# Kernel optimization log

Measured on AMD Instinct MI355X. Metric: run time of the kernel, lower is better.

Reference implementation:

```python
import jax, jax.numpy as jnp
import numpy as np

D_MODEL = 96
D_STATE = 6
D_CONV = 9
D_INNER = 2 * D_MODEL          # expand = 2
DT_RANK = (D_MODEL + 15) // 16  # ceil(d_model/16) = 6
DIM_IN = 64
DIM_OUT = 64
BATCH = 16
SEQLEN = 4096


def setup_inputs() -> dict:
    key = jax.random.key(0)
    ks = jax.random.split(key, 12)
    def s(k, shape, scale=0.02):
        return jax.random.normal(k, shape, jnp.float32) * scale
    return {
        "x": jax.random.normal(ks[0], (BATCH, SEQLEN, D_MODEL), jnp.float32),
        # Mamba block params
        "in_proj_w": s(ks[1], (2 * D_INNER, D_MODEL)),
        "conv_w": s(ks[2], (D_INNER, D_CONV), 0.1),   # depthwise conv kernel
        "conv_b": jnp.zeros((D_INNER,), jnp.float32),
        "x_proj_w": s(ks[3], (DT_RANK + 2 * D_STATE, D_INNER)),
        "dt_proj_w": s(ks[4], (D_INNER, DT_RANK), 0.1),
        "dt_proj_b": s(ks[5], (D_INNER,), 0.1),
        "A_log": jnp.log(jnp.tile(jnp.arange(1, D_STATE + 1, dtype=jnp.float32), (D_INNER, 1))),
        "D_param": jnp.ones((D_INNER,), jnp.float32),
        "out_proj_w": s(ks[6], (D_MODEL, D_INNER)),
        "norm_w": jnp.ones((D_MODEL,), jnp.float32),  # RMSNorm weight
        # heads
        "out_fc_w": s(ks[7], (DIM_IN, D_MODEL)),
        "out_fc_b": jnp.zeros((DIM_IN,), jnp.float32),
        "mu_w": s(ks[8], (DIM_OUT, DIM_IN)),
        "mu_b": jnp.zeros((DIM_OUT,), jnp.float32),
        "sigma_w": s(ks[9], (DIM_OUT, DIM_IN)),
        "sigma_b": jnp.zeros((DIM_OUT,), jnp.float32),
    }


def _mamba_block(x, in_proj_w, conv_w, conv_b, x_proj_w, dt_proj_w, dt_proj_b,
                 A_log, D_param, out_proj_w):
    Bsz = x.shape[0]
    xz = jnp.einsum('bld,ed->ble', x, in_proj_w)          # (B,L,2*ED)
    xs, z = jnp.split(xz, 2, axis=-1)
    # causal depthwise conv1d (torch pads d_conv-1 both sides then trims right)
    xt = xs.transpose(0, 2, 1)                            # (B,ED,L)
    kern = conv_w[:, None, :]                             # (ED,1,K)
    xc = jax.lax.conv_general_dilated(xt, kern, window_strides=(1,),
                                      padding=[(D_CONV - 1, 0)],
                                      feature_group_count=D_INNER)
    xc = (xc + conv_b[None, :, None]).transpose(0, 2, 1)  # (B,L,ED)
    xc = jax.nn.silu(xc)
    dbc = jnp.einsum('ble,fe->blf', xc, x_proj_w)         # (B,L,dt_rank+2N)
    delta_r = dbc[..., :DT_RANK]
    Bm = dbc[..., DT_RANK:DT_RANK + D_STATE]              # (B,L,N)
    Cm = dbc[..., DT_RANK + D_STATE:]                     # (B,L,N)
    delta = jax.nn.softplus(jnp.einsum('blr,er->ble', delta_r, dt_proj_w) + dt_proj_b)
    A = -jnp.exp(A_log)                                   # (ED,N)
    deltaA = jnp.exp(delta[..., None] * A)                # (B,L,ED,N)
    BX = (delta * xc)[..., None] * Bm[:, :, None, :]      # (B,L,ED,N)

    def step(h, inputs):
        dA, bx = inputs
        h = dA * h + bx
        return h, h

    h0 = jnp.zeros((Bsz, D_INNER, D_STATE), x.dtype)
    _, hs = jax.lax.scan(step, h0, (deltaA.swapaxes(0, 1), BX.swapaxes(0, 1)))
    y = jnp.einsum('lben,bln->ble', hs, Cm)               # (B,L,ED)
    y = y + D_param * xc
    y = y * jax.nn.silu(z)
    return jnp.einsum('ble,de->bld', y, out_proj_w)       # (B,L,D)


def reference(x, in_proj_w, conv_w, conv_b, x_proj_w, dt_proj_w, dt_proj_b,
              A_log, D_param, out_proj_w, norm_w,
              out_fc_w, out_fc_b, mu_w, mu_b, sigma_w, sigma_b):
    # residual block: x + mixer(RMSNorm(x))   (dropout is identity at eval)
    h = x * jax.lax.rsqrt(jnp.mean(x * x, axis=-1, keepdims=True) + 1e-5) * norm_w
    out = x + _mamba_block(h, in_proj_w, conv_w, conv_b, x_proj_w,
                           dt_proj_w, dt_proj_b, A_log, D_param, out_proj_w)
    e = out.mean(axis=1)                                  # (B,D)
    feat = jax.nn.elu(jnp.tanh(e @ out_fc_w.T + out_fc_b))
    mu = feat @ mu_w.T + mu_b
    sigma = jax.nn.elu(feat @ sigma_w.T + sigma_b) + 1.0 + 1e-14
    return (feat, mu, sigma)
```

## Files before the change

### kernel.cpp

```cpp
#include <hip/hip_runtime.h>
#include <math.h>

#define BATCH 16
#define SEQLEN 4096
#define D_MODEL 96
#define D_STATE 6
#define D_CONV 9
#define D_INNER 192
#define DT_RANK 6
#define NPOS (BATCH * SEQLEN)

#define NC2 128
#define CT2 (SEQLEN / NC2)
#define NSEG 16
#define CPS (NC2 / NSEG)

#define OFF_XS    0L
#define OFF_Z     (OFF_XS   + (long)NPOS * 96)
#define OFF_OUT4  (OFF_Z    + (long)NPOS * 96)
#define OFF_SEG   (OFF_OUT4 + (long)BATCH * NC2 * 5 * 192 * 4)
#define OFF_XPART (OFF_SEG  + (long)BATCH * NSEG * 5 * 192 * 4)

typedef short v8s __attribute__((ext_vector_type(8)));
typedef float v4f __attribute__((ext_vector_type(4)));

__device__ __forceinline__ float silu_fast(float v) {
    return __fdividef(v, 1.0f + __expf(-v));
}
__device__ __forceinline__ float softplus_fast(float v) {
    return (v > 20.0f) ? v : __logf(1.0f + __expf(v));
}
__device__ __forceinline__ float eluf(float v) {
    return (v > 0.0f) ? v : expm1f(v);
}
__device__ __forceinline__ unsigned int pack_bf16(float a, float b) {
    unsigned int ua = __float_as_uint(a), ub = __float_as_uint(b);
    ua += 0x7FFFu + ((ua >> 16) & 1u);
    ub += 0x7FFFu + ((ub >> 16) & 1u);
    return (ua >> 16) | (ub & 0xFFFF0000u);
}
__device__ __forceinline__ unsigned short bf16h(float v) {
    unsigned int u = __float_as_uint(v);
    u += 0x7FFFu + ((u >> 16) & 1u);
    return (unsigned short)(u >> 16);
}
__device__ __forceinline__ float bf2f(unsigned short h) {
    return __uint_as_float(((unsigned int)h) << 16);
}

#define TP1 64
__global__ __launch_bounds__(256, 2) void k1_rmsnorm_inproj(
    const float* __restrict__ x, const float* __restrict__ W,
    const float* __restrict__ norm_w,
    unsigned short* __restrict__ xs, unsigned short* __restrict__ z,
    float* __restrict__ xpart)
{
    __shared__ unsigned int s_ovl[7680];
    __shared__ unsigned int s_hA[64 * 52];
    __shared__ float s_part[TP1][4];
    __shared__ float s_scale[TP1];
    float* hRow = (float*)s_ovl;
    unsigned int* WB = s_ovl;

    const int tid = threadIdx.x;
    const long p0 = (long)blockIdx.x * TP1;

    {
        const float4* x4 = (const float4*)&x[p0 * 96];
        for (int i = tid; i < TP1 * 24; i += 256) {
            int p = i / 24, dq = i - p * 24;
            float4 v = x4[i];
            float* hr = &hRow[p * 101 + dq * 4];
            hr[0] = v.x; hr[1] = v.y; hr[2] = v.z; hr[3] = v.w;
        }
    }
    __syncthreads();

    {
        int p = tid >> 2, g = tid & 3;
        float ss = 0.0f;
        for (int d = g; d < 96; d += 4) { float v = hRow[p * 101 + d]; ss += v * v; }
        s_part[p][g] = ss;
    }
    __syncthreads();

    if (tid < TP1) {
        float ss = s_part[tid][0] + s_part[tid][1] + s_part[tid][2] + s_part[tid][3];
        s_scale[tid] = 1.0f / sqrtf(ss / 96.0f + 1e-5f);
    } else if (tid < TP1 + 96) {
        int d = tid - TP1;
        float s = 0.0f;
        for (int p = 0; p < TP1; p++) s += hRow[p * 101 + d];
        xpart[(long)blockIdx.x * 96 + d] = s;
    }
    __syncthreads();

    {
        const float2* nw2 = (const float2*)norm_w;
        for (int i = tid; i < TP1 * 48; i += 256) {
            int p = i / 48, dp = i - p * 48;
            float sc = s_scale[p];
            float2 nv = nw2[dp];
            float v0 = hRow[p * 101 + 2 * dp]     * sc * nv.x;
            float v1 = hRow[p * 101 + 2 * dp + 1] * sc * nv.y;
            s_hA[p * 52 + dp] = pack_bf16(v0, v1);
        }
    }
    __syncthreads();

    const int wave = tid >> 6, lane = tid & 63;
    const int quad = lane >> 4, ln = lane & 15;
    const int n0 = wave * 96;
    unsigned int* WBw = WB + wave * 1920;

    v4f acc[4][6];
#pragma unroll
    for (int mt = 0; mt < 4; mt++)
#pragma unroll
        for (int nt = 0; nt < 6; nt++) acc[mt][nt] = (v4f){0.f, 0.f, 0.f, 0.f};

    for (int kc = 0; kc < 3; kc++) {
#pragma unroll 8
        for (int ii = 0; ii < 24; ii++) {
            int i = lane + ii * 64;
            int jp = i >> 4, kp = i & 15;
            const float2 wv = *(const float2*)&W[(n0 + jp) * 96 + kc * 32 + 2 * kp];
            WBw[jp * 20 + kp] = pack_bf16(wv.x, wv.y);
        }
        v8s bfh[4];
#pragma unroll
        for (int mt = 0; mt < 4; mt++)
            bfh[mt] = *(const v8s*)&s_hA[(mt * 16 + ln) * 52 + kc * 16 + quad * 4];
#pragma unroll
        for (int nt = 0; nt < 6; nt++) {
            v8s aw = *(const v8s*)&WBw[(nt * 16 + ln) * 20 + quad * 4];
#pragma unroll
            for (int mt = 0; mt < 4; mt++)
                acc[mt][nt] = __builtin_amdgcn_mfma_f32_16x16x32_bf16(
                    aw, bfh[mt], acc[mt][nt], 0, 0, 0);
        }
    }

    unsigned short* dst = (wave < 2) ? xs : z;
    const int jb = (wave & 1) * 96;
#pragma unroll
    for (int mt = 0; mt < 4; mt++) {
        long pos = p0 + mt * 16 + ln;
#pragma unroll
        for (int nt = 0; nt < 6; nt++) {
            uint2 v;
            v.x = pack_bf16(acc[mt][nt][0], acc[mt][nt][1]);
            v.y = pack_bf16(acc[mt][nt][2], acc[mt][nt][3]);
            *(uint2*)&dst[pos * D_INNER + jb + nt * 16 + quad * 4] = v;
        }
    }
}

#define SXSTR 200
__global__ __launch_bounds__(192, 4) void k2f_conv_scan(
    const unsigned short* __restrict__ xs, const unsigned short* __restrict__ z,
    const float* __restrict__ conv_w, const float* __restrict__ conv_b,
    const float* __restrict__ x_proj_w,
    const float* __restrict__ dt_w, const float* __restrict__ dt_b,
    const float* __restrict__ A_log, const float* __restrict__ D_param,
    float4* __restrict__ out4)
{
    __shared__ unsigned short sxc[CT2 * SXSTR];
    __shared__ unsigned short sxpB[18 * SXSTR];
    __shared__ float sMeta[CT2][20];
    const int e = threadIdx.x;
    const int c = blockIdx.x & (NC2 - 1);
    const int b = blockIdx.x >> 7;
    const int l0 = c * CT2;
    const long brow = (long)b * SEQLEN;

    {
        unsigned int* xpB = (unsigned int*)sxpB;
        for (int i = e; i < 18 * 96; i += 192) {
            int f = i / 96, kp = i - f * 96;
            const float2 wv = *(const float2*)&x_proj_w[f * 192 + 2 * kp];
            xpB[f * 100 + kp] = pack_bf16(wv.x, wv.y);
        }
    }

    float cw[D_CONV];
#pragma unroll
    for (int k = 0; k < D_CONV; k++) cw[k] = conv_w[e * D_CONV + k];
    const float cb = conv_b[e];
    float win[D_CONV];
#pragma unroll
    for (int k = 0; k < 8; k++) {
        int ll = l0 - 8 + k;
        win[k] = (ll >= 0) ? bf2f(xs[(brow + ll) * D_INNER + e]) : 0.0f;
    }
#pragma unroll
    for (int r = 0; r < CT2; r++) {
        win[8] = bf2f(xs[(brow + l0 + r) * D_INNER + e]);
        float s = cb;
#pragma unroll
        for (int k = 0; k < D_CONV; k++) s += win[k] * cw[k];
        sxc[r * SXSTR + e] = bf16h(silu_fast(s));
#pragma unroll
        for (int k = 0; k < 8; k++) win[k] = win[k + 1];
    }

    const unsigned short* zp = &z[(brow + l0) * D_INNER + e];
    float zv[CT2];
#pragma unroll
    for (int t = 0; t < CT2; t++) zv[t] = bf2f(zp[(long)t * D_INNER]);
    __syncthreads();

    {
        const int wave = e >> 6, lane = e & 63;
        const int quad = lane >> 4, ln = lane & 15;
        if (wave < 2) {
            const int mt = wave;
            const int r1 = (ln < 2) ? 16 + ln : 0;
            v4f dacc[2];
            dacc[0] = (v4f){0.f, 0.f, 0.f, 0.f};
            dacc[1] = (v4f){0.f, 0.f, 0.f, 0.f};
#pragma unroll
            for (int kc = 0; kc < 6; kc++) {
                v8s af  = *(const v8s*)&sxc[(mt * 16 + ln) * SXSTR + kc * 32 + quad * 8];
                v8s bf0 = *(const v8s*)&sxpB[ln * SXSTR + kc * 32 + quad * 8];
                v8s bf1 = *(const v8s*)&sxpB[r1 * SXSTR + kc * 32 + quad * 8];
                dacc[0] = __builtin_amdgcn_mfma_f32_16x16x32_bf16(af, bf0, dacc[0], 0, 0, 0);
                dacc[1] = __builtin_amdgcn_mfma_f32_16x16x32_bf16(af, bf1, dacc[1], 0, 0, 0);
            }
#pragma unroll
            for (int nt = 0; nt < 2; nt++) {
                int f = nt * 16 + ln;
                if (f < 18) {
                    int col = (f < 6) ? f : f + 2;
#pragma unroll
                    for (int r = 0; r < 4; r++)
                        sMeta[mt * 16 + quad * 4 + r][col] = dacc[nt][r];
                }
            }
        }
    }
    __syncthreads();

    float a[D_STATE];
#pragma unroll
    for (int n = 0; n < D_STATE; n++) a[n] = -__expf(A_log[e * D_STATE + n]);
    float dtw[DT_RANK];
#pragma unroll
    for (int q = 0; q < DT_RANK; q++) dtw[q] = dt_w[e * DT_RANK + q];
    const float dtb = dt_b[e];
    const float Dv = D_param[e];
    const float a0 = a[0];

    bool pok = true;
#pragma unroll
    for (int n = 1; n < D_STATE; n++)
        pok = pok && (fabsf(a[n] - (float)(n + 1) * a0)
                      <= 1e-4f * (float)(n + 1) * fabsf(a0));
    unsigned long long pmask = __ballot(pok);

    float S[D_STATE], G[D_STATE];
#pragma unroll
    for (int n = 0; n < D_STATE; n++) { S[n] = 0.0f; G[n] = 0.0f; }
    float ysum0 = 0.0f;

    if (pmask == 0xFFFFFFFFFFFFFFFFull) {
        float Pa = 1.0f;
#pragma unroll 2
        for (int t = 0; t < CT2; t++) {
            const float4* m4 = (const float4*)&sMeta[t][0];
            float4 m0 = m4[0], m1 = m4[1], mB0 = m4[2], mB1 = m4[3], mC = m4[4];
            float Bv[6] = {mB0.x, mB0.y, mB0.z, mB0.w, mB1.x, mB1.y};
            float Cv[6] = {mB1.z, mB1.w, mC.x, mC.y, mC.z, mC.w};
            float dr = dtb + m0.x * dtw[0] + m0.y * dtw[1] + m0.z * dtw[2]
                     + m0.w * dtw[3] + m1.x * dtw[4] + m1.y * dtw[5];
            float dl = softplus_fast(dr);
            float xv = bf2f(sxc[t * SXSTR + e]);
            float zw = silu_fast(zv[t]);
            float dx = dl * xv;
            float y = Dv * xv;
            float E = __expf(dl * a0);
            Pa *= E;
            float dA = E, Pn = Pa;
#pragma unroll
            for (int n = 0; n < D_STATE; n++) {
                S[n] = dA * S[n] + dx * Bv[n];
                y += S[n] * Cv[n];
                G[n] += zw * Pn * Cv[n];
                dA *= E;
                Pn *= Pa;
            }
            ysum0 += zw * y;
        }
        long ob = (long)(b * NC2 + c) * 5 * 192 + e;
        float P1 = Pa, P2 = P1 * Pa, P3 = P2 * Pa, P4 = P3 * Pa, P5 = P4 * Pa, P6 = P5 * Pa;
        float4 q0, q1, q2, q3, q4;
        q0.x=P1; q0.y=P2; q0.z=P3; q0.w=P4;
        q1.x=P5; q1.y=P6; q1.z=S[0]; q1.w=S[1];
        q2.x=S[2]; q2.y=S[3]; q2.z=S[4]; q2.w=S[5];
        q3.x=G[0]; q3.y=G[1]; q3.z=G[2]; q3.w=G[3];
        q4.x=G[4]; q4.y=G[5]; q4.z=ysum0; q4.w=0.0f;
        out4[ob          ] = q0;
        out4[ob + 192    ] = q1;
        out4[ob + 2 * 192] = q2;
        out4[ob + 3 * 192] = q3;
        out4[ob + 4 * 192] = q4;
    } else {
        float P[D_STATE];
#pragma unroll
        for (int n = 0; n < D_STATE; n++) P[n] = 1.0f;
#pragma unroll 2
        for (int t = 0; t < CT2; t++) {
            const float4* m4 = (const float4*)&sMeta[t][0];
            float4 m0 = m4[0], m1 = m4[1], mB0 = m4[2], mB1 = m4[3], mC = m4[4];
            float Bv[6] = {mB0.x, mB0.y, mB0.z, mB0.w, mB1.x, mB1.y};
            float Cv[6] = {mB1.z, mB1.w, mC.x, mC.y, mC.z, mC.w};
            float dr = dtb + m0.x * dtw[0] + m0.y * dtw[1] + m0.z * dtw[2]
                     + m0.w * dtw[3] + m1.x * dtw[4] + m1.y * dtw[5];
            float dl = softplus_fast(dr);
            float xv = bf2f(sxc[t * SXSTR + e]);
            float zw = silu_fast(zv[t]);
            float dx = dl * xv;
            float y = Dv * xv;
#pragma unroll
            for (int n = 0; n < D_STATE; n++) {
                float dA = __expf(dl * a[n]);
                S[n] = dA * S[n] + dx * Bv[n];
                P[n] *= dA;
                y += S[n] * Cv[n];
                G[n] += zw * P[n] * Cv[n];
            }
            ysum0 += zw * y;
        }
        long ob = (long)(b * NC2 + c) * 5 * 192 + e;
        float4 q0, q1, q2, q3, q4;
        q0.x=P[0]; q0.y=P[1]; q0.z=P[2]; q0.w=P[3];
        q1.x=P[4]; q1.y=P[5]; q1.z=S[0]; q1.w=S[1];
        q2.x=S[2]; q2.y=S[3]; q2.z=S[4]; q2.w=S[5];
        q3.x=G[0]; q3.y=G[1]; q3.z=G[2]; q3.w=G[3];
        q4.x=G[4]; q4.y=G[5]; q4.z=ysum0; q4.w=0.0f;
        out4[ob          ] = q0;
        out4[ob + 192    ] = q1;
        out4[ob + 2 * 192] = q2;
        out4[ob + 3 * 192] = q3;
        out4[ob + 4 * 192] = q4;
    }
}

__global__ __launch_bounds__(192) void k4_seg(
    const float4* __restrict__ out4, float4* __restrict__ seg4)
{
    const int e = threadIdx.x;
    const int s = blockIdx.x & (NSEG - 1);
    const int b = blockIdx.x >> 4;

    float H[D_STATE], Gq[D_STATE], Pp[D_STATE];
#pragma unroll
    for (int n = 0; n < D_STATE; n++) { H[n] = 0.0f; Gq[n] = 0.0f; Pp[n] = 1.0f; }
    float yb = 0.0f;
#pragma unroll 2
    for (int cc = 0; cc < CPS; cc++) {
        int c = s * CPS + cc;
        long ob = (long)(b * NC2 + c) * 5 * 192 + e;
        float4 q0 = out4[ob];
        float4 q1 = out4[ob + 192];
        float4 q2 = out4[ob + 2 * 192];
        float4 q3 = out4[ob + 3 * 192];
        float4 q4 = out4[ob + 4 * 192];
        float Pv[6] = {q0.x, q0.y, q0.z, q0.w, q1.x, q1.y};
        float Sv[6] = {q1.z, q1.w, q2.x, q2.y, q2.z, q2.w};
        float Gv[6] = {q3.x, q3.y, q3.z, q3.w, q4.x, q4.y};
        float g = 0.0f;
#pragma unroll
        for (int n = 0; n < D_STATE; n++) g += Gv[n] * H[n];
        yb += q4.z + g;
#pragma unroll
        for (int n = 0; n < D_STATE; n++) {
            Gq[n] += Gv[n] * Pp[n];
            H[n] = Pv[n] * H[n] + Sv[n];
            Pp[n] *= Pv[n];
        }
    }
    long sb = (long)(b * NSEG + s) * 5 * 192 + e;
    float4 q0, q1, q2, q3, q4;
    q0.x=Pp[0]; q0.y=Pp[1]; q0.z=Pp[2]; q0.w=Pp[3];
    q1.x=Pp[4]; q1.y=Pp[5]; q1.z=H[0]; q1.w=H[1];
    q2.x=H[2]; q2.y=H[3]; q2.z=H[4]; q2.w=H[5];
    q3.x=Gq[0]; q3.y=Gq[1]; q3.z=Gq[2]; q3.w=Gq[3];
    q4.x=Gq[4]; q4.y=Gq[5]; q4.z=yb; q4.w=0.0f;
    seg4[sb          ] = q0;
    seg4[sb + 192    ] = q1;
    seg4[sb + 2 * 192] = q2;
    seg4[sb + 3 * 192] = q3;
    seg4[sb + 4 * 192] = q4;
}

__global__ __launch_bounds__(192) void k4_head(
    const float4* __restrict__ seg4, const float* __restrict__ xpart,
    const float* __restrict__ Wout,
    const float* __restrict__ fc_w, const float* __restrict__ fc_b,
    const float* __restrict__ mu_w, const float* __restrict__ mu_b,
    const float* __restrict__ sg_w, const float* __restrict__ sg_b,
    float* __restrict__ out)
{
    __shared__ float ybar[D_INNER];
    __shared__ float sxb[D_MODEL];
    __shared__ float evec[D_MODEL];
    __shared__ float feat_s[64];
    const int e = threadIdx.x;
    const int b = blockIdx.x;

    float H[D_STATE];
#pragma unroll
    for (int n = 0; n < D_STATE; n++) H[n] = 0.0f;
    float yb = 0.0f;
#pragma unroll 4
    for (int s = 0; s < NSEG; s++) {
        long ob = (long)(b * NSEG + s) * 5 * 192 + e;
        float4 q0 = seg4[ob];
        float4 q1 = seg4[ob + 192];
        float4 q2 = seg4[ob + 2 * 192];
        float4 q3 = seg4[ob + 3 * 192];
        float4 q4 = seg4[ob + 4 * 192];
        float Pv[6] = {q0.x, q0.y, q0.z, q0.w, q1.x, q1.y};
        float Sv[6] = {q1.z, q1.w, q2.x, q2.y, q2.z, q2.w};
        float Gv[6] = {q3.x, q3.y, q3.z, q3.w, q4.x, q4.y};
        float g = 0.0f;
#pragma unroll
        for (int n = 0; n < D_STATE; n++) g += Gv[n] * H[n];
        yb += q4.z + g;
#pragma unroll
        for (int n = 0; n < D_STATE; n++) H[n] = Pv[n] * H[n] + Sv[n];
    }
    ybar[e] = yb;

    if (e < D_MODEL) {
        const float* xp = &xpart[(long)b * 64 * 96 + e];
        float s = 0.0f;
        for (int t = 0; t < 64; t++) s += xp[t * 96];
        sxb[e] = s;
    }
    __syncthreads();

    if (e < D_MODEL) {
        float s = sxb[e];
        const float* wrow = &Wout[e * D_INNER];
        for (int e2 = 0; e2 < D_INNER; e2++) s += ybar[e2] * wrow[e2];
        evec[e] = s / (float)SEQLEN;
    }
    __syncthreads();

    if (e < 64) {
        float s = fc_b[e];
        const float* wrow = &fc_w[e * D_MODEL];
        for (int d = 0; d < D_MODEL; d++) s += evec[d] * wrow[d];
        float f = eluf(tanhf(s));
        feat_s[e] = f;
        out[b * 64 + e] = f;
    }
    __syncthreads();

    if (e < 64) {
        float smu = mu_b[e], ssg = sg_b[e];
        const float* mrow = &mu_w[e * 64];
        const float* srow = &sg_w[e * 64];
        for (int i = 0; i < 64; i++) {
            smu += feat_s[i] * mrow[i];
            ssg += feat_s[i] * srow[i];
        }
        out[1024 + b * 64 + e] = smu;
        out[2048 + b * 64 + e] = eluf(ssg) + 1.0f + 1e-14f;
    }
}

extern "C" void kernel_launch(void* const* d_in, const int* in_sizes, int n_in,
                              void* d_out, int out_size, void* d_ws, size_t ws_size,
                              hipStream_t stream) {
    const float* x         = (const float*)d_in[0];
    const float* in_proj_w = (const float*)d_in[1];
    const float* conv_w    = (const float*)d_in[2];
    const float* conv_b    = (const float*)d_in[3];
    const float* x_proj_w  = (const float*)d_in[4];
    const float* dt_proj_w = (const float*)d_in[5];
    const float* dt_proj_b = (const float*)d_in[6];
    const float* A_log     = (const float*)d_in[7];
    const float* D_param   = (const float*)d_in[8];
    const float* out_proj_w= (const float*)d_in[9];
    const float* norm_w    = (const float*)d_in[10];
    const float* out_fc_w  = (const float*)d_in[11];
    const float* out_fc_b  = (const float*)d_in[12];
    const float* mu_w      = (const float*)d_in[13];
    const float* mu_b      = (const float*)d_in[14];
    const float* sigma_w   = (const float*)d_in[15];
    const float* sigma_b   = (const float*)d_in[16];
    float* ws = (float*)d_ws;
    float* out = (float*)d_out;

    k1_rmsnorm_inproj<<<NPOS / TP1, 256, 0, stream>>>(
        x, in_proj_w, norm_w,
        (unsigned short*)(ws + OFF_XS), (unsigned short*)(ws + OFF_Z),
        ws + OFF_XPART);

    k2f_conv_scan<<<BATCH * NC2, 192, 0, stream>>>(
        (const unsigned short*)(ws + OFF_XS), (const unsigned short*)(ws + OFF_Z),
        conv_w, conv_b, x_proj_w,
        dt_proj_w, dt_proj_b, A_log, D_param,
        (float4*)(ws + OFF_OUT4));

    k4_seg<<<BATCH * NSEG, 192, 0, stream>>>(
        (const float4*)(ws + OFF_OUT4), (float4*)(ws + OFF_SEG));

    k4_head<<<BATCH, 192, 0, stream>>>(
        (const float4*)(ws + OFF_SEG), ws + OFF_XPART, out_proj_w,
        out_fc_w, out_fc_b, mu_w, mu_b, sigma_w, sigma_b, out);
}
```

Measured before the change: 201.1 us.

## Fuse silu(z) into in_proj epilogue, prepack x_proj weights, restructure scan loop

Applies silu to z in the in_proj kernel's epilogue before the bf16 store, so the scan kernel no longer evaluates silu per step. The x_proj weights are packed to bf16 once by block 0 of the first kernel into workspace, and the scan kernel reads MFMA operands straight from global memory instead of repacking them into shared memory in every block. The fast-path scan is split into two halves of 16 steps: a first pass computes the exp, dt*x and z terms, and a second pass does the serial recurrence. The D*x contribution is also pulled out of the per-step sum. z values are now loaded inside the loop rather than preloaded into registers, and bf16 rounding after silu slightly changes numerics.

Result: slower. 269.8 us (+34.2%).

```diff
diff --git a/kernel.cpp b/kernel.cpp
--- a/kernel.cpp
+++ b/kernel.cpp
@@ -20,6 +20,7 @@
 #define OFF_OUT4  (OFF_Z    + (long)NPOS * 96)
 #define OFF_SEG   (OFF_OUT4 + (long)BATCH * NC2 * 5 * 192 * 4)
 #define OFF_XPART (OFF_SEG  + (long)BATCH * NSEG * 5 * 192 * 4)
+#define OFF_XPB   (OFF_XPART + (long)(NPOS / 64) * 96)
 
 typedef short v8s __attribute__((ext_vector_type(8)));
 typedef float v4f __attribute__((ext_vector_type(4)));
@@ -51,9 +52,9 @@
 #define TP1 64
 __global__ __launch_bounds__(256, 2) void k1_rmsnorm_inproj(
     const float* __restrict__ x, const float* __restrict__ W,
-    const float* __restrict__ norm_w,
+    const float* __restrict__ norm_w, const float* __restrict__ x_proj_w,
     unsigned short* __restrict__ xs, unsigned short* __restrict__ z,
-    float* __restrict__ xpart)
+    float* __restrict__ xpart, unsigned int* __restrict__ xpb)
 {
     __shared__ unsigned int s_ovl[7680];
     __shared__ unsigned int s_hA[64 * 52];
@@ -142,16 +143,30 @@
     }
 
     unsigned short* dst = (wave < 2) ? xs : z;
+    const bool is_z = (wave >= 2);
     const int jb = (wave & 1) * 96;
 #pragma unroll
     for (int mt = 0; mt < 4; mt++) {
         long pos = p0 + mt * 16 + ln;
 #pragma unroll
         for (int nt = 0; nt < 6; nt++) {
+            float f0 = acc[mt][nt][0], f1 = acc[mt][nt][1];
+            float f2 = acc[mt][nt][2], f3 = acc[mt][nt][3];
+            if (is_z) {
+                f0 = silu_fast(f0); f1 = silu_fast(f1);
+                f2 = silu_fast(f2); f3 = silu_fast(f3);
+            }
             uint2 v;
-            v.x = pack_bf16(acc[mt][nt][0], acc[mt][nt][1]);
-            v.y = pack_bf16(acc[mt][nt][2], acc[mt][nt][3]);
+            v.x = pack_bf16(f0, f1);
+            v.y = pack_bf16(f2, f3);
             *(uint2*)&dst[pos * D_INNER + jb + nt * 16 + quad * 4] = v;
+        }
+    }
+
+    if (blockIdx.x == 0) {
+        for (int i = tid; i < 18 * 96; i += 256) {
+            const float2 wv = *(const float2*)&x_proj_w[2 * i];
+            xpb[i] = pack_bf16(wv.x, wv.y);
         }
     }
 }
@@ -160,13 +175,12 @@
 __global__ __launch_bounds__(192, 4) void k2f_conv_scan(
     const unsigned short* __restrict__ xs, const unsigned short* __restrict__ z,
     const float* __restrict__ conv_w, const float* __restrict__ conv_b,
-    const float* __restrict__ x_proj_w,
+    const unsigned short* __restrict__ xpb,
     const float* __restrict__ dt_w, const float* __restrict__ dt_b,
     const float* __restrict__ A_log, const float* __restrict__ D_param,
     float4* __restrict__ out4)
 {
     __shared__ unsigned short sxc[CT2 * SXSTR];
-    __shared__ unsigned short sxpB[18 * SXSTR];
     __shared__ float sMeta[CT2][20];
     const int e = threadIdx.x;
     const int c = blockIdx.x & (NC2 - 1);
@@ -174,15 +188,6 @@
     const int l0 = c * CT2;
     const long brow = (long)b * SEQLEN;
 
-    {
-        unsigned int* xpB = (unsigned int*)sxpB;
-        for (int i = e; i < 18 * 96; i += 192) {
-            int f = i / 96, kp = i - f * 96;
-            const float2 wv = *(const float2*)&x_proj_w[f * 192 + 2 * kp];
-            xpB[f * 100 + kp] = pack_bf16(wv.x, wv.y);
-        }
-    }
-
     float cw[D_CONV];
 #pragma unroll
     for (int k = 0; k < D_CONV; k++) cw[k] = conv_w[e * D_CONV + k];
@@ -205,9 +210,6 @@
     }
 
     const unsigned short* zp = &z[(brow + l0) * D_INNER + e];
-    float zv[CT2];
-#pragma unroll
-    for (int t = 0; t < CT2; t++) zv[t] = bf2f(zp[(long)t * D_INNER]);
     __syncthreads();
 
     {
@@ -222,8 +224,8 @@
 #pragma unroll
             for (int kc = 0; kc < 6; kc++) {
                 v8s af  = *(const v8s*)&sxc[(mt * 16 + ln) * SXSTR + kc * 32 + quad * 8];
-                v8s bf0 = *(const v8s*)&sxpB[ln * SXSTR + kc * 32 + quad * 8];
-                v8s bf1 = *(const v8s*)&sxpB[r1 * SXSTR + kc * 32 + quad * 8];
+                v8s bf0 = *(const v8s*)&xpb[ln * 192 + kc * 32 + quad * 8];
+                v8s bf1 = *(const v8s*)&xpb[r1 * 192 + kc * 32 + quad * 8];
                 dacc[0] = __builtin_amdgcn_mfma_f32_16x16x32_bf16(af, bf0, dacc[0], 0, 0, 0);
                 dacc[1] = __builtin_amdgcn_mfma_f32_16x16x32_bf16(af, bf1, dacc[1], 0, 0, 0);
             }
@@ -265,32 +267,48 @@
 
     if (pmask == 0xFFFFFFFFFFFFFFFFull) {
         float Pa = 1.0f;
-#pragma unroll 2
-        for (int t = 0; t < CT2; t++) {
-            const float4* m4 = (const float4*)&sMeta[t][0];
-            float4 m0 = m4[0], m1 = m4[1], mB0 = m4[2], mB1 = m4[3], mC = m4[4];
-            float Bv[6] = {mB0.x, mB0.y, mB0.z, mB0.w, mB1.x, mB1.y};
-            float Cv[6] = {mB1.z, mB1.w, mC.x, mC.y, mC.z, mC.w};
-            float dr = dtb + m0.x * dtw[0] + m0.y * dtw[1] + m0.z * dtw[2]
-                     + m0.w * dtw[3] + m1.x * dtw[4] + m1.y * dtw[5];
-            float dl = softplus_fast(dr);
-            float xv = bf2f(sxc[t * SXSTR + e]);
-            float zw = silu_fast(zv[t]);
-            float dx = dl * xv;
-            float y = Dv * xv;
-            float E = __expf(dl * a0);
-            Pa *= E;
-            float dA = E, Pn = Pa;
-#pragma unroll
-            for (int n = 0; n < D_STATE; n++) {
-                S[n] = dA * S[n] + dx * Bv[n];
-                y += S[n] * Cv[n];
-                G[n] += zw * Pn * Cv[n];
-                dA *= E;
-                Pn *= Pa;
+        float ysumA = 0.0f;
+#pragma unroll
+        for (int h = 0; h < 2; h++) {
+            const int t0 = h * 16;
+            float E_[16], dx_[16], zw_[16];
+#pragma unroll
+            for (int tt = 0; tt < 16; tt++) {
+                const float4* m4 = (const float4*)&sMeta[t0 + tt][0];
+                float4 m0 = m4[0], m1 = m4[1];
+                float dr = dtb + m0.x * dtw[0] + m0.y * dtw[1] + m0.z * dtw[2]
+                         + m0.w * dtw[3] + m1.x * dtw[4] + m1.y * dtw[5];
+                float dl = softplus_fast(dr);
+                float xv = bf2f(sxc[(t0 + tt) * SXSTR + e]);
+                float zwv = bf2f(zp[(long)(t0 + tt) * D_INNER]);
+                E_[tt] = __expf(dl * a0);
+                dx_[tt] = dl * xv;
+                zw_[tt] = zwv;
+                ysumA += zwv * xv;
             }
-            ysum0 += zw * y;
-        }
+#pragma unroll
+            for (int tt = 0; tt < 16; tt++) {
+                const float4* m4 = (const float4*)&sMeta[t0 + tt][0];
+                float4 mB0 = m4[2], mB1 = m4[3], mC = m4[4];
+                float Bv[6] = {mB0.x, mB0.y, mB0.z, mB0.w, mB1.x, mB1.y};
+                float Cv[6] = {mB1.z, mB1.w, mC.x, mC.y, mC.z, mC.w};
+                float E = E_[tt], dxv = dx_[tt], zwv = zw_[tt];
+                Pa *= E;
+                float dA = E;
+                float w = zwv * Pa;
+                float y = 0.0f;
+#pragma unroll
+                for (int n = 0; n < D_STATE; n++) {
+                    S[n] = dA * S[n] + dxv * Bv[n];
+                    y += S[n] * Cv[n];
+                    G[n] += w * Cv[n];
+                    dA *= E;
+                    w *= Pa;
+                }
+                ysum0 += zwv * y;
+            }
+        }
+        ysum0 += Dv * ysumA;
         long ob = (long)(b * NC2 + c) * 5 * 192 + e;
         float P1 = Pa, P2 = P1 * Pa, P3 = P2 * Pa, P4 = P3 * Pa, P5 = P4 * Pa, P6 = P5 * Pa;
         float4 q0, q1, q2, q3, q4;
@@ -318,7 +336,7 @@
                      + m0.w * dtw[3] + m1.x * dtw[4] + m1.y * dtw[5];
             float dl = softplus_fast(dr);
             float xv = bf2f(sxc[t * SXSTR + e]);
-            float zw = silu_fast(zv[t]);
+            float zw = bf2f(zp[(long)t * D_INNER]);
             float dx = dl * xv;
             float y = Dv * xv;
 #pragma unroll
@@ -496,13 +514,13 @@
     float* out = (float*)d_out;
 
     k1_rmsnorm_inproj<<<NPOS / TP1, 256, 0, stream>>>(
-        x, in_proj_w, norm_w,
+        x, in_proj_w, norm_w, x_proj_w,
         (unsigned short*)(ws + OFF_XS), (unsigned short*)(ws + OFF_Z),
-        ws + OFF_XPART);
+        ws + OFF_XPART, (unsigned int*)(ws + OFF_XPB));
 
     k2f_conv_scan<<<BATCH * NC2, 192, 0, stream>>>(
         (const unsigned short*)(ws + OFF_XS), (const unsigned short*)(ws + OFF_Z),
-        conv_w, conv_b, x_proj_w,
+        conv_w, conv_b, (const unsigned short*)(ws + OFF_XPB),
         dt_proj_w, dt_proj_b, A_log, D_param,
         (float4*)(ws + OFF_OUT4));
 
```
